# Performance work log

Measured on AMD Instinct MI355X. Metric: run time of the kernel, lower is better.

Reference implementation:

```python
import jax, jax.numpy as jnp
import numpy as np

CE_WEIGHT = 1.0
TRIPLET_WEIGHT = 0.1
MARGIN = 0.2


def setup_inputs() -> dict:
    key = jax.random.key(0)
    k1, k2, k3 = jax.random.split(key, 3)
    B, D, V = 4096, 512, 6000
    logits = jax.random.normal(k1, (B, V), dtype=jnp.float32)
    embeddings = jax.random.normal(k2, (B, D), dtype=jnp.float32)
    labels = jax.random.randint(k3, (B,), 0, 512, dtype=jnp.int64)
    return {"logits": logits, "embeddings": embeddings, "labels": labels}


def _pairwise_dist(emb):
    # Euclidean cdist via gram matrix; safe sqrt (zero grad where d2 == 0).
    sq = jnp.sum(emb * emb, axis=-1)  # [B]
    d2 = sq[:, None] + sq[None, :] - 2.0 * (emb @ emb.T)  # [B, B]
    d2 = jnp.maximum(d2, 0.0)
    safe = jnp.where(d2 > 0.0, d2, 1.0)
    return jnp.where(d2 > 0.0, jnp.sqrt(safe), 0.0)


def _losses(logits, embeddings, labels):
    B = logits.shape[0]
    # Cross entropy (mean reduction, matching nn.CrossEntropyLoss).
    logp = jax.nn.log_softmax(logits, axis=-1)
    ce_loss = -jnp.mean(jnp.take_along_axis(logp, labels[:, None], axis=1)[:, 0])

    # Batch-hard triplet loss, fully vectorized (one masked amax/amin per row).
    dist = _pairwise_dist(embeddings)  # [B, B]
    same = labels[:, None] == labels[None, :]  # [B, B]
    eye = jnp.eye(B, dtype=bool)
    pos_mask = same & ~eye
    neg_mask = ~same
    neg_inf = jnp.float32(-np.inf)
    pos_inf = jnp.float32(np.inf)
    hardest_pos = jnp.max(jnp.where(pos_mask, dist, neg_inf), axis=1)  # [B]
    hardest_neg = jnp.min(jnp.where(neg_mask, dist, pos_inf), axis=1)  # [B]
    valid = jnp.any(pos_mask, axis=1) & jnp.any(neg_mask, axis=1)  # [B]
    per_row = jax.nn.relu(hardest_pos - hardest_neg + MARGIN)
    per_row = jnp.where(valid, per_row, 0.0)
    n_valid = jnp.sum(valid.astype(jnp.float32))
    triplet_loss = jnp.where(n_valid > 0, jnp.sum(per_row) / jnp.maximum(n_valid, 1.0), 0.0)

    total_loss = CE_WEIGHT * ce_loss + TRIPLET_WEIGHT * triplet_loss
    return total_loss, ce_loss, triplet_loss


def reference(logits, embeddings, labels):
    return _losses(logits, embeddings, labels)
```

## Files before the change

### kernel.cpp

```cpp
#include <hip/hip_runtime.h>
#include <hip/hip_bf16.h>
#include <math.h>

#define BN   4096
#define DN   512
#define VN   6000
#define NCLS 512

typedef __attribute__((ext_vector_type(8)))  short short8;
typedef __attribute__((ext_vector_type(16))) float f32x16;

__device__ __forceinline__ unsigned short f2bf(float x) {
  unsigned int u = __float_as_uint(x);
  u = (u + 0x7FFFu + ((u >> 16) & 1u)) >> 16;
  return (unsigned short)u;
}

__device__ __forceinline__ void gld_lds16(const unsigned short* g, unsigned short* l) {
  __builtin_amdgcn_global_load_lds(
      (const __attribute__((address_space(1))) void*)g,
      (__attribute__((address_space(3))) void*)l, 16, 0, 0);
}

__launch_bounds__(256)
__global__ void prep_kernel(const float* __restrict__ emb, const int* __restrict__ labels,
                            unsigned short* __restrict__ embh, float* __restrict__ sqn,
                            int* __restrict__ cnt, int* __restrict__ posb,
                            int* __restrict__ negb) {
  const int row  = blockIdx.x * 4 + (threadIdx.x >> 6);
  const int lane = threadIdx.x & 63;
  const float4* rp = (const float4*)(emb + (size_t)row * DN);
  float4 a = rp[lane];
  float4 b = rp[lane + 64];
  float ss = a.x * a.x + a.y * a.y + a.z * a.z + a.w * a.w
           + b.x * b.x + b.y * b.y + b.z * b.z + b.w * b.w;
  ushort4 ha, hb;
  ha.x = f2bf(a.x); ha.y = f2bf(a.y); ha.z = f2bf(a.z); ha.w = f2bf(a.w);
  hb.x = f2bf(b.x); hb.y = f2bf(b.y); hb.z = f2bf(b.z); hb.w = f2bf(b.w);
  ushort4* wp = (ushort4*)(embh + (size_t)row * DN);
  wp[lane] = ha;
  wp[lane + 64] = hb;
#pragma unroll
  for (int off = 1; off < 64; off <<= 1) ss += __shfl_xor(ss, off);
  if (lane == 0) {
    sqn[row] = ss;
    posb[row] = 0;
    negb[row] = 0x7F800000;
    atomicAdd(cnt + labels[row], 1);
  }
}

__device__ __forceinline__ void trip128(int t, unsigned short* smem,
                                        const unsigned short* __restrict__ embh,
                                        const float* __restrict__ sqn,
                                        const int* __restrict__ labels,
                                        int* __restrict__ posb,
                                        int* __restrict__ negb, int tid) {
  const int lane = tid & 63;
  const int w    = tid >> 6;
  const int wi   = w >> 1;
  const int wj   = w & 1;
  const int m    = lane & 31;
  const int half = lane >> 5;

  int J = (int)((sqrtf(8.f * (float)t + 1.f) - 1.f) * 0.5f);
  while ((J + 1) * (J + 2) / 2 <= t) ++J;
  while (J * (J + 1) / 2 > t) --J;
  const int I = t - J * (J + 1) / 2;
  const int i0 = I * 128, j0 = J * 128;
  const bool qdiag = (I == J) && (wi == wj);

  const int   side = tid >> 7;
  const int   idx  = tid & 127;
  const int   grow = (side ? j0 : i0) + idx;
  const int   lme  = labels[grow];
  const float qme  = sqn[grow];

  const int lrow = lane >> 3;
  const int lchk = (lane & 7) ^ lrow;
  const int prow = w * 8 + lrow;
  const unsigned short* gA = embh + (size_t)(i0 + prow) * DN + lchk * 8;
  const unsigned short* gB = embh + (size_t)(j0 + prow) * DN + lchk * 8;

#define TJ_STAGE(bufoff, kk)                                                  \
  do {                                                                        \
    _Pragma("unroll")                                                         \
    for (int s = 0; s < 4; ++s)                                               \
      gld_lds16(gA + (kk) + (size_t)s * 32 * DN,                              \
                smem + (bufoff) + (s * 32 + w * 8) * 64);                     \
    _Pragma("unroll")                                                         \
    for (int s = 0; s < 4; ++s)                                               \
      gld_lds16(gB + (kk) + (size_t)s * 32 * DN,                              \
                smem + (bufoff) + 8192 + (s * 32 + w * 8) * 64);              \
  } while (0)

  f32x16 acc[2][2] = {};
  f32x16 accT[2][2] = {};

  TJ_STAGE(0, 0);

#pragma unroll
  for (int ks = 0; ks < 8; ++ks) {
    const int cur = (ks & 1) * 16384;
    asm volatile("s_waitcnt lgkmcnt(0)" ::: "memory");
    __builtin_amdgcn_s_barrier();
    if (ks < 7) {
      TJ_STAGE(16384 - cur, (ks + 1) * 64);
      asm volatile("s_waitcnt vmcnt(8)" ::: "memory");
    } else {
      asm volatile("s_waitcnt vmcnt(0)" ::: "memory");
    }
    __builtin_amdgcn_s_barrier();
    const unsigned short* sA = smem + cur;
    const unsigned short* sB = smem + cur + 8192;
#pragma unroll
    for (int q = 0; q < 4; ++q) {
      const int c = q * 2 + half;
      const int sw = (c ^ (m & 7)) * 8;
      short8 a0 = *(const short8*)&sA[(wi * 64 + m) * 64 + sw];
      short8 a1 = *(const short8*)&sA[(wi * 64 + 32 + m) * 64 + sw];
      short8 b0 = *(const short8*)&sB[(wj * 64 + m) * 64 + sw];
      short8 b1 = *(const short8*)&sB[(wj * 64 + 32 + m) * 64 + sw];
      acc[0][0]  = __builtin_amdgcn_mfma_f32_32x32x16_bf16(a0, b0, acc[0][0], 0, 0, 0);
      acc[0][1]  = __builtin_amdgcn_mfma_f32_32x32x16_bf16(a0, b1, acc[0][1], 0, 0, 0);
      acc[1][0]  = __builtin_amdgcn_mfma_f32_32x32x16_bf16(a1, b0, acc[1][0], 0, 0, 0);
      acc[1][1]  = __builtin_amdgcn_mfma_f32_32x32x16_bf16(a1, b1, acc[1][1], 0, 0, 0);
      accT[0][0] = __builtin_amdgcn_mfma_f32_32x32x16_bf16(b0, a0, accT[0][0], 0, 0, 0);
      accT[0][1] = __builtin_amdgcn_mfma_f32_32x32x16_bf16(b0, a1, accT[0][1], 0, 0, 0);
      accT[1][0] = __builtin_amdgcn_mfma_f32_32x32x16_bf16(b1, a0, accT[1][0], 0, 0, 0);
      accT[1][1] = __builtin_amdgcn_mfma_f32_32x32x16_bf16(b1, a1, accT[1][1], 0, 0, 0);
    }
  }
#undef TJ_STAGE

  int*   sLab = (int*)smem;
  float* sQn  = (float*)(smem + 512);
  sLab[tid] = lme;
  sQn[tid]  = qme;
  __syncthreads();

  {
    const int jb  = 128 + wj * 64;
    const int gj0 = j0 + wj * 64 + m, gj1 = gj0 + 32;
    const int cl0 = sLab[jb + m], cl1 = sLab[jb + 32 + m];
    const float cq0 = sQn[jb + m], cq1 = sQn[jb + 32 + m];
    float p0 = 0.f, p1 = 0.f, n0 = INFINITY, n1 = INFINITY;
#pragma unroll
    for (int rb = 0; rb < 2; ++rb) {
#pragma unroll
      for (int r = 0; r < 16; ++r) {
        const int ri = wi * 64 + rb * 32 + (r & 3) + 8 * (r >> 2) + 4 * half;
        const int gi = i0 + ri;
        const int rl = sLab[ri];
        const float rq = sQn[ri];
        const float d0 = fmaf(-2.f, acc[rb][0][r], rq + cq0);
        const float d1 = fmaf(-2.f, acc[rb][1][r], rq + cq1);
        if (rl == cl0) { if (gi != gj0) p0 = fmaxf(p0, d0); } else n0 = fminf(n0, d0);
        if (rl == cl1) { if (gi != gj1) p1 = fmaxf(p1, d1); } else n1 = fminf(n1, d1);
      }
    }
    p0 = fmaxf(p0, __shfl_xor(p0, 32)); n0 = fminf(n0, __shfl_xor(n0, 32));
    p1 = fmaxf(p1, __shfl_xor(p1, 32)); n1 = fminf(n1, __shfl_xor(n1, 32));
    if (half == 0) {
      atomicMax(posb + gj0, __float_as_int(p0));
      atomicMin(negb + gj0, __float_as_int(n0));
      atomicMax(posb + gj1, __float_as_int(p1));
      atomicMin(negb + gj1, __float_as_int(n1));
    }
  }

  if (!qdiag) {
    const int gj0 = i0 + wi * 64 + m, gj1 = gj0 + 32;
    const int cl0 = sLab[wi * 64 + m], cl1 = sLab[wi * 64 + 32 + m];
    const float cq0 = sQn[wi * 64 + m], cq1 = sQn[wi * 64 + 32 + m];
    float p0 = 0.f, p1 = 0.f, n0 = INFINITY, n1 = INFINITY;
#pragma unroll
    for (int rb = 0; rb < 2; ++rb) {
#pragma unroll
      for (int r = 0; r < 16; ++r) {
        const int rj = wj * 64 + rb * 32 + (r & 3) + 8 * (r >> 2) + 4 * half;
        const int rl = sLab[128 + rj];
        const float rq = sQn[128 + rj];
        const float d0 = fmaf(-2.f, accT[rb][0][r], rq + cq0);
        const float d1 = fmaf(-2.f, accT[rb][1][r], rq + cq1);
        if (rl == cl0) p0 = fmaxf(p0, d0); else n0 = fminf(n0, d0);
        if (rl == cl1) p1 = fmaxf(p1, d1); else n1 = fminf(n1, d1);
      }
    }
    p0 = fmaxf(p0, __shfl_xor(p0, 32)); n0 = fminf(n0, __shfl_xor(n0, 32));
    p1 = fmaxf(p1, __shfl_xor(p1, 32)); n1 = fminf(n1, __shfl_xor(n1, 32));
    if (half == 0) {
      atomicMax(posb + gj0, __float_as_int(p0));
      atomicMin(negb + gj0, __float_as_int(n0));
      atomicMax(posb + gj1, __float_as_int(p1));
      atomicMin(negb + gj1, __float_as_int(n1));
    }
  }
}

__launch_bounds__(256, 2)
__global__ void fused_kernel(const float* __restrict__ logits,
                             const int* __restrict__ labels,
                             float* __restrict__ ce_part,
                             const unsigned short* __restrict__ embh,
                             const float* __restrict__ sqn,
                             int* __restrict__ posb, int* __restrict__ negb) {
  __shared__ unsigned short smem[32768];
  const int b = blockIdx.x;
  const int tid = threadIdx.x;

  int trip_job, ce_base;
  if (b < 16) {
    trip_job = 512 + b; ce_base = -1;
  } else {
    const int g = (b - 16) / 3, r = (b - 16) % 3;
    if (r == 0) { trip_job = g; ce_base = -1; }
    else        { trip_job = -1; ce_base = (g * 2 + (r - 1)) * 4; }
  }

  if (trip_job >= 0) {
    trip128(trip_job, smem, embh, sqn, labels, posb, negb, tid);
    return;
  }

  const int ce_row = ce_base + (tid >> 6);
  const int lane = tid & 63;
  const float* rp = logits + (size_t)ce_row * VN;
  const float xlab = rp[labels[ce_row]];
  const float4* q = (const float4*)rp;
  float4 v[24];
#pragma unroll
  for (int u = 0; u < 23; ++u) v[u] = q[lane + u * 64];
  if (lane < 28) v[23] = q[lane + 23 * 64];
  float s = 0.f;
#pragma unroll
  for (int u = 0; u < 23; ++u)
    s += __expf(v[u].x) + __expf(v[u].y) + __expf(v[u].z) + __expf(v[u].w);
  if (lane < 28)
    s += __expf(v[23].x) + __expf(v[23].y) + __expf(v[23].z) + __expf(v[23].w);
#pragma unroll
  for (int off = 1; off < 64; off <<= 1) s += __shfl_xor(s, off);
  if (lane == 0) ce_part[ce_row] = logf(s) - xlab;
}

__launch_bounds__(1024)
__global__ void finalize_kernel(const int* __restrict__ posb, const int* __restrict__ negb,
                                const int* __restrict__ labels, const int* __restrict__ cnt,
                                const float* __restrict__ ce_part, float* __restrict__ out) {
  const int tid = threadIdx.x;
  float cesum = 0.f, sum = 0.f, nv = 0.f;
#pragma unroll
  for (int u = 0; u < 4; ++u) {
    const int i = tid + u * 1024;
    cesum += ce_part[i];
    int c = cnt[labels[i]];
    float p = sqrtf(fmaxf(__int_as_float(posb[i]), 0.f));
    float n = sqrtf(fmaxf(__int_as_float(negb[i]), 0.f));
    float t = fmaxf(p - n + 0.2f, 0.f);
    if (c >= 2 && c < BN) { sum += t; nv += 1.f; }
  }
#pragma unroll
  for (int off = 1; off < 64; off <<= 1) {
    cesum += __shfl_xor(cesum, off);
    sum   += __shfl_xor(sum, off);
    nv    += __shfl_xor(nv, off);
  }
  __shared__ float s0[16], s1[16], s2[16];
  if ((tid & 63) == 0) { s0[tid >> 6] = cesum; s1[tid >> 6] = sum; s2[tid >> 6] = nv; }
  __syncthreads();
  if (tid == 0) {
    cesum = 0.f; sum = 0.f; nv = 0.f;
#pragma unroll
    for (int wv = 0; wv < 16; ++wv) { cesum += s0[wv]; sum += s1[wv]; nv += s2[wv]; }
    float trip = (nv > 0.f) ? sum / nv : 0.f;
    float ce = cesum * (1.f / BN);
    out[0] = ce + 0.1f * trip;
    out[1] = ce;
    out[2] = trip;
  }
}

extern "C" void kernel_launch(void* const* d_in, const int* in_sizes, int n_in,
                              void* d_out, int out_size, void* d_ws, size_t ws_size,
                              hipStream_t stream) {
  const float* logits = (const float*)d_in[0];
  const float* emb    = (const float*)d_in[1];
  const int*   labels = (const int*)d_in[2];
  float* out = (float*)d_out;

  char* ws = (char*)d_ws;
  unsigned short* embh = (unsigned short*)ws;
  float* sqn    = (float*)(ws + (size_t)BN * DN * 2);
  int*   posb   = (int*)((char*)sqn  + (size_t)BN * 4);
  int*   negb   = (int*)((char*)posb + (size_t)BN * 4);
  int*   cnt    = (int*)((char*)negb + (size_t)BN * 4);
  float* ce_part = (float*)((char*)cnt + (size_t)NCLS * 4);

  hipMemsetAsync(cnt, 0, (size_t)NCLS * 4, stream);
  hipLaunchKernelGGL(prep_kernel, dim3(BN / 4), dim3(256), 0, stream,
                     emb, labels, embh, sqn, cnt, posb, negb);
  hipLaunchKernelGGL(fused_kernel, dim3(16 + 512 * 3), dim3(256), 0, stream,
                     logits, labels, ce_part, embh, sqn, posb, negb);
  hipLaunchKernelGGL(finalize_kernel, dim3(1), dim3(1024), 0, stream,
                     posb, negb, labels, cnt, ce_part, out);
}
```

Measured before the change: 171.6 us.

## Split fused triplet/CE kernel into separate sequential kernels

Replaces the single fused kernel, which interleaved triplet gram-tile blocks with cross-entropy blocks in one grid, with two kernels launched back to back: one for the 528 triplet tiles and one for the 1024 cross-entropy blocks. This removes the block-index dispatch logic and stops the CE blocks from paying for the large shared-memory allocation and register budget of the triplet path. In exchange, the memory-bound CE work can no longer overlap with the compute-bound triplet work, and there is an extra launch.

```diff
diff --git a/kernel.cpp b/kernel.cpp
--- a/kernel.cpp
+++ b/kernel.cpp
@@ -199,32 +199,20 @@
 }
 
 __launch_bounds__(256, 2)
-__global__ void fused_kernel(const float* __restrict__ logits,
-                             const int* __restrict__ labels,
-                             float* __restrict__ ce_part,
-                             const unsigned short* __restrict__ embh,
-                             const float* __restrict__ sqn,
-                             int* __restrict__ posb, int* __restrict__ negb) {
+__global__ void trip_kernel(const unsigned short* __restrict__ embh,
+                            const float* __restrict__ sqn,
+                            const int* __restrict__ labels,
+                            int* __restrict__ posb, int* __restrict__ negb) {
   __shared__ unsigned short smem[32768];
-  const int b = blockIdx.x;
-  const int tid = threadIdx.x;
-
-  int trip_job, ce_base;
-  if (b < 16) {
-    trip_job = 512 + b; ce_base = -1;
-  } else {
-    const int g = (b - 16) / 3, r = (b - 16) % 3;
-    if (r == 0) { trip_job = g; ce_base = -1; }
-    else        { trip_job = -1; ce_base = (g * 2 + (r - 1)) * 4; }
-  }
-
-  if (trip_job >= 0) {
-    trip128(trip_job, smem, embh, sqn, labels, posb, negb, tid);
-    return;
-  }
-
-  const int ce_row = ce_base + (tid >> 6);
-  const int lane = tid & 63;
+  trip128(blockIdx.x, smem, embh, sqn, labels, posb, negb, threadIdx.x);
+}
+
+__launch_bounds__(256, 2)
+__global__ void ce_kernel(const float* __restrict__ logits,
+                          const int* __restrict__ labels,
+                          float* __restrict__ ce_part) {
+  const int ce_row = blockIdx.x * 4 + (threadIdx.x >> 6);
+  const int lane = threadIdx.x & 63;
   const float* rp = logits + (size_t)ce_row * VN;
   const float xlab = rp[labels[ce_row]];
   const float4* q = (const float4*)rp;
@@ -299,8 +287,10 @@
   hipMemsetAsync(cnt, 0, (size_t)NCLS * 4, stream);
   hipLaunchKernelGGL(prep_kernel, dim3(BN / 4), dim3(256), 0, stream,
                      emb, labels, embh, sqn, cnt, posb, negb);
-  hipLaunchKernelGGL(fused_kernel, dim3(16 + 512 * 3), dim3(256), 0, stream,
-                     logits, labels, ce_part, embh, sqn, posb, negb);
+  hipLaunchKernelGGL(trip_kernel, dim3(528), dim3(256), 0, stream,
+                     embh, sqn, labels, posb, negb);
+  hipLaunchKernelGGL(ce_kernel, dim3(BN / 4), dim3(256), 0, stream,
+                     logits, labels, ce_part);
   hipLaunchKernelGGL(finalize_kernel, dim3(1), dim3(1024), 0, stream,
                      posb, negb, labels, cnt, ce_part, out);
 }
```

Measured after the change: 187.9 us. 9.5% more time.

## Replace global atomic max/min with per-slab partial buffers and separate reduce kernel

Applied to the files above, without the earlier changes.

Triplet tiles no longer fold their per-column hardest-positive and hardest-negative values into global arrays with atomicMax and atomicMin. Each tile instead writes plain stores into a 64-slab partial buffer indexed by tile row-half, and a new reduce kernel collapses the slabs before finalize. This removes atomic contention and the init stores in prep. The cost is an extra kernel launch and about 2 MB of partial-buffer traffic. The diagonal-quadrant handling now relies on slab indexing, so every slab entry must be written for correctness.

```diff
diff --git a/kernel.cpp b/kernel.cpp
--- a/kernel.cpp
+++ b/kernel.cpp
@@ -25,8 +25,7 @@
 __launch_bounds__(256)
 __global__ void prep_kernel(const float* __restrict__ emb, const int* __restrict__ labels,
                             unsigned short* __restrict__ embh, float* __restrict__ sqn,
-                            int* __restrict__ cnt, int* __restrict__ posb,
-                            int* __restrict__ negb) {
+                            int* __restrict__ cnt) {
   const int row  = blockIdx.x * 4 + (threadIdx.x >> 6);
   const int lane = threadIdx.x & 63;
   const float4* rp = (const float4*)(emb + (size_t)row * DN);
@@ -44,8 +43,6 @@
   for (int off = 1; off < 64; off <<= 1) ss += __shfl_xor(ss, off);
   if (lane == 0) {
     sqn[row] = ss;
-    posb[row] = 0;
-    negb[row] = 0x7F800000;
     atomicAdd(cnt + labels[row], 1);
   }
 }
@@ -54,8 +51,8 @@
                                         const unsigned short* __restrict__ embh,
                                         const float* __restrict__ sqn,
                                         const int* __restrict__ labels,
-                                        int* __restrict__ posb,
-                                        int* __restrict__ negb, int tid) {
+                                        float* __restrict__ pp,
+                                        float* __restrict__ nn, int tid) {
   const int lane = tid & 63;
   const int w    = tid >> 6;
   const int wi   = w >> 1;
@@ -68,7 +65,6 @@
   while (J * (J + 1) / 2 > t) --J;
   const int I = t - J * (J + 1) / 2;
   const int i0 = I * 128, j0 = J * 128;
-  const bool qdiag = (I == J) && (wi == wj);
 
   const int   side = tid >> 7;
   const int   idx  = tid & 127;
@@ -162,14 +158,13 @@
     p0 = fmaxf(p0, __shfl_xor(p0, 32)); n0 = fminf(n0, __shfl_xor(n0, 32));
     p1 = fmaxf(p1, __shfl_xor(p1, 32)); n1 = fminf(n1, __shfl_xor(n1, 32));
     if (half == 0) {
-      atomicMax(posb + gj0, __float_as_int(p0));
-      atomicMin(negb + gj0, __float_as_int(n0));
-      atomicMax(posb + gj1, __float_as_int(p1));
-      atomicMin(negb + gj1, __float_as_int(n1));
-    }
-  }
-
-  if (!qdiag) {
+      const size_t sb = (size_t)(I * 2 + wi) * BN;
+      pp[sb + gj0] = p0;  nn[sb + gj0] = n0;
+      pp[sb + gj1] = p1;  nn[sb + gj1] = n1;
+    }
+  }
+
+  if (I != J) {
     const int gj0 = i0 + wi * 64 + m, gj1 = gj0 + 32;
     const int cl0 = sLab[wi * 64 + m], cl1 = sLab[wi * 64 + 32 + m];
     const float cq0 = sQn[wi * 64 + m], cq1 = sQn[wi * 64 + 32 + m];
@@ -190,10 +185,9 @@
     p0 = fmaxf(p0, __shfl_xor(p0, 32)); n0 = fminf(n0, __shfl_xor(n0, 32));
     p1 = fmaxf(p1, __shfl_xor(p1, 32)); n1 = fminf(n1, __shfl_xor(n1, 32));
     if (half == 0) {
-      atomicMax(posb + gj0, __float_as_int(p0));
-      atomicMin(negb + gj0, __float_as_int(n0));
-      atomicMax(posb + gj1, __float_as_int(p1));
-      atomicMin(negb + gj1, __float_as_int(n1));
+      const size_t sb = (size_t)(J * 2 + wj) * BN;
+      pp[sb + gj0] = p0;  nn[sb + gj0] = n0;
+      pp[sb + gj1] = p1;  nn[sb + gj1] = n1;
     }
   }
 }
@@ -204,7 +198,7 @@
                              float* __restrict__ ce_part,
                              const unsigned short* __restrict__ embh,
                              const float* __restrict__ sqn,
-                             int* __restrict__ posb, int* __restrict__ negb) {
+                             float* __restrict__ pp, float* __restrict__ nn) {
   __shared__ unsigned short smem[32768];
   const int b = blockIdx.x;
   const int tid = threadIdx.x;
@@ -219,7 +213,7 @@
   }
 
   if (trip_job >= 0) {
-    trip128(trip_job, smem, embh, sqn, labels, posb, negb, tid);
+    trip128(trip_job, smem, embh, sqn, labels, pp, nn, tid);
     return;
   }
 
@@ -243,8 +237,22 @@
   if (lane == 0) ce_part[ce_row] = logf(s) - xlab;
 }
 
+__launch_bounds__(256)
+__global__ void reduce_kernel(const float* __restrict__ pp, const float* __restrict__ nn,
+                              float* __restrict__ hp, float* __restrict__ hn) {
+  const int row = blockIdx.x * 256 + threadIdx.x;
+  float p = 0.f, n = INFINITY;
+#pragma unroll
+  for (int s = 0; s < 64; ++s) {
+    p = fmaxf(p, pp[(size_t)s * BN + row]);
+    n = fminf(n, nn[(size_t)s * BN + row]);
+  }
+  hp[row] = p;
+  hn[row] = n;
+}
+
 __launch_bounds__(1024)
-__global__ void finalize_kernel(const int* __restrict__ posb, const int* __restrict__ negb,
+__global__ void finalize_kernel(const float* __restrict__ hp, const float* __restrict__ hn,
                                 const int* __restrict__ labels, const int* __restrict__ cnt,
                                 const float* __restrict__ ce_part, float* __restrict__ out) {
   const int tid = threadIdx.x;
@@ -254,8 +262,8 @@
     const int i = tid + u * 1024;
     cesum += ce_part[i];
     int c = cnt[labels[i]];
-    float p = sqrtf(fmaxf(__int_as_float(posb[i]), 0.f));
-    float n = sqrtf(fmaxf(__int_as_float(negb[i]), 0.f));
+    float p = sqrtf(fmaxf(hp[i], 0.f));
+    float n = sqrtf(fmaxf(hn[i], 0.f));
     float t = fmaxf(p - n + 0.2f, 0.f);
     if (c >= 2 && c < BN) { sum += t; nv += 1.f; }
   }
@@ -290,17 +298,21 @@
 
   char* ws = (char*)d_ws;
   unsigned short* embh = (unsigned short*)ws;
-  float* sqn    = (float*)(ws + (size_t)BN * DN * 2);
-  int*   posb   = (int*)((char*)sqn  + (size_t)BN * 4);
-  int*   negb   = (int*)((char*)posb + (size_t)BN * 4);
-  int*   cnt    = (int*)((char*)negb + (size_t)BN * 4);
+  float* sqn     = (float*)(ws + (size_t)BN * DN * 2);
+  int*   cnt     = (int*)((char*)sqn  + (size_t)BN * 4);
   float* ce_part = (float*)((char*)cnt + (size_t)NCLS * 4);
+  float* pp      = (float*)((char*)ce_part + (size_t)BN * 4);
+  float* nn      = (float*)((char*)pp + (size_t)64 * BN * 4);
+  float* hp      = (float*)((char*)nn + (size_t)64 * BN * 4);
+  float* hn      = (float*)((char*)hp + (size_t)BN * 4);
 
   hipMemsetAsync(cnt, 0, (size_t)NCLS * 4, stream);
   hipLaunchKernelGGL(prep_kernel, dim3(BN / 4), dim3(256), 0, stream,
-                     emb, labels, embh, sqn, cnt, posb, negb);
+                     emb, labels, embh, sqn, cnt);
   hipLaunchKernelGGL(fused_kernel, dim3(16 + 512 * 3), dim3(256), 0, stream,
-                     logits, labels, ce_part, embh, sqn, posb, negb);
+                     logits, labels, ce_part, embh, sqn, pp, nn);
+  hipLaunchKernelGGL(reduce_kernel, dim3(BN / 256), dim3(256), 0, stream,
+                     pp, nn, hp, hn);
   hipLaunchKernelGGL(finalize_kernel, dim3(1), dim3(1024), 0, stream,
-                     posb, negb, labels, cnt, ce_part, out);
-}
+                     hp, hn, labels, cnt, ce_part, out);
+}
```

After: 191.1 us. 11.3% more time.
